# Kernel tuning notes

Hardware: AMD Instinct MI355X
Metric: run time of the kernel (lower is better)

The kernel has to match this reference:

```python
import jax, jax.numpy as jnp
import numpy as np

N = 100_000
E = 1_600_000
H = 128
L = 3
EPS = 1e-5


def setup_inputs() -> dict:
    key = jax.random.key(0)
    ks = jax.random.split(key, 8)
    x = jax.random.normal(ks[0], (N, H), dtype=jnp.float32)
    edge_index = jax.random.randint(ks[1], (2, E), 0, N, dtype=jnp.int64)
    edge_weight = jax.random.uniform(ks[2], (E,), dtype=jnp.float32)
    # per-layer params (all layers are H->H since in_dim == hidden)
    s = 1.0 / np.sqrt(H)
    lin_neigh_w = jax.random.uniform(ks[3], (L, H, H), minval=-s, maxval=s, dtype=jnp.float32)
    lin_root_w = jax.random.uniform(ks[4], (L, H, H), minval=-s, maxval=s, dtype=jnp.float32)
    lin_root_b = jax.random.uniform(ks[5], (L, H), minval=-s, maxval=s, dtype=jnp.float32)
    ln_w = jnp.ones((L, H), dtype=jnp.float32)
    ln_b = jnp.zeros((L, H), dtype=jnp.float32)
    return {"x": x, "edge_index": edge_index, "edge_weight": edge_weight,
            "lin_neigh_w": lin_neigh_w, "lin_root_w": lin_root_w,
            "lin_root_b": lin_root_b, "ln_w": ln_w, "ln_b": ln_b}


def _layer(h, src, dst, e_w, w_neigh, w_root, b_root, g, b):
    # message: m_ij = w_ij * x_j ; aggregate: scatter-add over dst, normalized by sum of weights
    msg = e_w[:, None] * h[src]                                    # [E, H]
    agg = jax.ops.segment_sum(msg, dst, num_segments=N)            # [N, H]
    sum_w = jnp.clip(jax.ops.segment_sum(e_w, dst, num_segments=N), 1.0, None)
    out = agg / sum_w[:, None]
    out = out @ w_neigh.T + h @ w_root.T + b_root                  # lin_neigh + lin_root
    out = jax.nn.relu(out)
    # per-node LayerNorm over feature dim
    mu = jnp.mean(out, axis=-1, keepdims=True)
    var = jnp.var(out, axis=-1, keepdims=True)
    out = (out - mu) * jax.lax.rsqrt(var + EPS) * g + b
    return out  # dropout: inference no-op


def reference(x, edge_index, edge_weight, lin_neigh_w, lin_root_w, lin_root_b, ln_w, ln_b):
    src, dst = edge_index[0], edge_index[1]
    h = x
    for l in range(L):
        h = _layer(h, src, dst, edge_weight, lin_neigh_w[l], lin_root_w[l],
                   lin_root_b[l], ln_w[l], ln_b[l])
    return h
```

## Files before the change

kernel.cpp:

```cpp
#include <hip/hip_runtime.h>
#include <hip/hip_fp16.h>

#define H 128
#define EPS 1e-5f
#define BCAP 6144

typedef __attribute__((ext_vector_type(8))) _Float16 half8;
typedef __attribute__((ext_vector_type(4))) float f32x4;

__device__ inline __half2 u2h2(unsigned u) { return __builtin_bit_cast(__half2, u); }
__device__ inline unsigned h22u(__half2 h) { return __builtin_bit_cast(unsigned, h); }

__global__ void convert_kernel(const float* __restrict__ x, unsigned* __restrict__ hx, int n4) {
    int i = blockIdx.x * 256 + threadIdx.x;
    if (i >= n4) return;
    float4 v = reinterpret_cast<const float4*>(x)[i];
    unsigned p0 = h22u(__floats2half2_rn(v.x, v.y));
    unsigned p1 = h22u(__floats2half2_rn(v.z, v.w));
    reinterpret_cast<uint2*>(hx)[i] = make_uint2(p0, p1);
}

__global__ __launch_bounds__(256) void bhist_kernel(const int* __restrict__ dst,
                                                    int* __restrict__ ghist, int E, int NB) {
    __shared__ int hist[512];
    int t = threadIdx.x;
    for (int i = t; i < NB; i += 256) hist[i] = 0;
    __syncthreads();
    int base = blockIdx.x * 8192 + t;
#pragma unroll
    for (int k = 0; k < 32; ++k) {
        int e = base + k * 256;
        if (e < E) atomicAdd(&hist[dst[e] >> 8], 1);
    }
    __syncthreads();
    for (int i = t; i < NB; i += 256)
        if (hist[i]) atomicAdd(&ghist[i], hist[i]);
}

__global__ __launch_bounds__(512) void bscan_kernel(const int* __restrict__ ghist,
                                                    int* __restrict__ bucket_base,
                                                    int* __restrict__ cursor,
                                                    int* __restrict__ row_start,
                                                    int NB, int E, int N) {
    __shared__ int lds[512];
    int t = threadIdx.x;
    int v = (t < NB) ? ghist[t] : 0;
    lds[t] = v;
    __syncthreads();
    for (int off = 1; off < 512; off <<= 1) {
        int u = (t >= off) ? lds[t - off] : 0;
        __syncthreads();
        lds[t] += u;
        __syncthreads();
    }
    int excl = lds[t] - v;
    if (t < NB) {
        bucket_base[t] = excl;
        cursor[t] = excl;
    }
    if (t == 0) {
        bucket_base[NB] = E;
        row_start[N] = E;
    }
}

__global__ __launch_bounds__(1024) void bucketize_kernel(const int* __restrict__ src,
                                                         const int* __restrict__ dst,
                                                         const float* __restrict__ ew,
                                                         int* __restrict__ cursor,
                                                         int2* __restrict__ ee, int E, int NB) {
    __shared__ int hist[512];
    __shared__ int scn[512];
    __shared__ int gbase[512];
    __shared__ int2 stage[8192];
    int t = threadIdx.x;
    for (int i = t; i < NB; i += 1024) hist[i] = 0;
    __syncthreads();

    int e0 = blockIdx.x * 8192;
    int bb[8], rk[8], pk[8], wb[8];
#pragma unroll
    for (int k = 0; k < 8; ++k) {
        int e = e0 + t + k * 1024;
        if (e < E) {
            int s = src[e], d = dst[e];
            bb[k] = d >> 8;
            pk[k] = s | ((d & 255) << 17);
            wb[k] = __float_as_int(ew[e]);
            rk[k] = atomicAdd(&hist[bb[k]], 1);
        } else {
            bb[k] = -1;
        }
    }
    __syncthreads();
    if (t < 512) scn[t] = (t < NB) ? hist[t] : 0;
    __syncthreads();
    for (int off = 1; off < 512; off <<= 1) {
        int u = 0;
        if (t < 512 && t >= off) u = scn[t - off];
        __syncthreads();
        if (t < 512) scn[t] += u;
        __syncthreads();
    }
    for (int i = t; i < NB; i += 1024) {
        int c = hist[i];
        if (c > 0) gbase[i] = atomicAdd(&cursor[i], c);
    }
#pragma unroll
    for (int k = 0; k < 8; ++k) {
        if (bb[k] >= 0) {
            int start = scn[bb[k]] - hist[bb[k]];
            stage[start + rk[k]] = make_int2(pk[k], wb[k]);
        }
    }
    __syncthreads();
    int wv = t >> 6, ln = t & 63;
    for (int bk = wv; bk < NB; bk += 16) {
        int c = hist[bk];
        if (c == 0) continue;
        int s0 = scn[bk] - c;
        int gb = gbase[bk];
        for (int i = ln; i < c; i += 64) ee[gb + i] = stage[s0 + i];
    }
}

__global__ __launch_bounds__(256) void bsort_kernel(int2* __restrict__ ee,
                                                    const int* __restrict__ bucket_base,
                                                    int* __restrict__ row_start, int N) {
    __shared__ int cnts[256];
    __shared__ int scv[256];
    __shared__ int prefs[256];
    __shared__ int2 out[BCAP];
    int b = blockIdx.x;
    int base = bucket_base[b], endb = bucket_base[b + 1];
    int cnt = endb - base;
    int t = threadIdx.x;
    cnts[t] = 0;
    __syncthreads();
    for (int i = base + t; i < endb; i += 256) atomicAdd(&cnts[(ee[i].x >> 17) & 255], 1);
    __syncthreads();
    scv[t] = cnts[t];
    __syncthreads();
    for (int off = 1; off < 256; off <<= 1) {
        int u = (t >= off) ? scv[t - off] : 0;
        __syncthreads();
        scv[t] += u;
        __syncthreads();
    }
    int pref = scv[t] - cnts[t];
    prefs[t] = pref;
    int node = (b << 8) + t;
    if (node < N) row_start[node] = base + pref;
    __syncthreads();
    cnts[t] = 0;
    __syncthreads();
    for (int i = base + t; i < endb; i += 256) {
        int2 r = ee[i];
        int dl = (r.x >> 17) & 255;
        int rkk = atomicAdd(&cnts[dl], 1);
        int slot = prefs[dl] + rkk;
        if (slot < BCAP) out[slot] = make_int2(r.x & 0x1FFFF, r.y);
    }
    __syncthreads();
    {
        int s0 = prefs[t], c = cnts[t];
        float sw = 0.f;
        for (int k = 0; k < c; ++k) sw += __int_as_float(out[s0 + k].y);
        sw = sw < 1.f ? 1.f : sw;
        float inv = 1.f / sw;
        for (int k = 0; k < c; ++k) {
            float w = __int_as_float(out[s0 + k].y) * inv;
            unsigned hb = (unsigned)__half_as_ushort(__float2half(w));
            out[s0 + k].y = (int)(hb | (hb << 16));
        }
    }
    __syncthreads();
    for (int i = t; i < cnt; i += 256) ee[base + i] = out[i];
}

__global__ __launch_bounds__(256) void agg_kernel(const unsigned short* __restrict__ hx,
                                                  const int* __restrict__ row_start,
                                                  const int2* __restrict__ ee,
                                                  unsigned short* __restrict__ aggb, int N) {
    int t = threadIdx.x;
    int node = blockIdx.x * 4 + (t >> 6);
    if (node >= N) return;
    int lane = t & 63, q = lane >> 4, jb = lane & 15;
    unsigned acc0 = 0, acc1 = 0, acc2 = 0, acc3 = 0;
    __half2 h0 = u2h2(0), h1 = u2h2(0), h2 = u2h2(0), h3 = u2h2(0);
    int rs = row_start[node], re = row_start[node + 1];
    int i = rs;
    for (; i + 8 <= re; i += 8) {
        int2 ea = ee[i + q];
        int2 eb = ee[i + 4 + q];
        uint4 ua = *reinterpret_cast<const uint4*>(hx + (size_t)ea.x * H + jb * 8);
        uint4 ub = *reinterpret_cast<const uint4*>(hx + (size_t)eb.x * H + jb * 8);
        __half2 wa = u2h2((unsigned)ea.y), wb = u2h2((unsigned)eb.y);
        h0 = __hfma2(u2h2(ua.x), wa, h0);
        h1 = __hfma2(u2h2(ua.y), wa, h1);
        h2 = __hfma2(u2h2(ua.z), wa, h2);
        h3 = __hfma2(u2h2(ua.w), wa, h3);
        h0 = __hfma2(u2h2(ub.x), wb, h0);
        h1 = __hfma2(u2h2(ub.y), wb, h1);
        h2 = __hfma2(u2h2(ub.z), wb, h2);
        h3 = __hfma2(u2h2(ub.w), wb, h3);
    }
    for (; i < re; i += 4) {
        int idx = i + q;
        int2 ea = (idx < re) ? ee[idx] : make_int2(0, 0);
        uint4 ua = *reinterpret_cast<const uint4*>(hx + (size_t)ea.x * H + jb * 8);
        __half2 wa = u2h2((unsigned)ea.y);
        h0 = __hfma2(u2h2(ua.x), wa, h0);
        h1 = __hfma2(u2h2(ua.y), wa, h1);
        h2 = __hfma2(u2h2(ua.z), wa, h2);
        h3 = __hfma2(u2h2(ua.w), wa, h3);
    }
    acc0 = h22u(h0); acc1 = h22u(h1); acc2 = h22u(h2); acc3 = h22u(h3);
#pragma unroll
    for (int off = 16; off <= 32; off <<= 1) {
        acc0 = h22u(__hadd2(u2h2(acc0), u2h2((unsigned)__shfl_xor((int)acc0, off))));
        acc1 = h22u(__hadd2(u2h2(acc1), u2h2((unsigned)__shfl_xor((int)acc1, off))));
        acc2 = h22u(__hadd2(u2h2(acc2), u2h2((unsigned)__shfl_xor((int)acc2, off))));
        acc3 = h22u(__hadd2(u2h2(acc3), u2h2((unsigned)__shfl_xor((int)acc3, off))));
    }
    if (q == 0) {
        uint4 r = make_uint4(acc0, acc1, acc2, acc3);
        *reinterpret_cast<uint4*>(aggb + (size_t)node * H + jb * 8) = r;
    }
}

__global__ __launch_bounds__(256, 2) void gemm_ln_mfma(
    const unsigned short* __restrict__ aggb, const unsigned short* __restrict__ hx,
    const float* __restrict__ Wn, const float* __restrict__ Wr,
    const float* __restrict__ br, const float* __restrict__ g,
    const float* __restrict__ b, unsigned short* __restrict__ hout,
    float* __restrict__ outf, int final_layer, int N) {
    __shared__ half8 Bfl[4096];

    int t = threadIdx.x;
    int w = t >> 6, lane = t & 63;
    int Mbase = blockIdx.x * 256;

#pragma unroll
    for (int it = 0; it < 16; ++it) {
        int f = it * 4 + w;
        int kt = f >> 3, nb = f & 7;
        int n = nb * 16 + (lane & 15);
        int kk = (kt & 3) * 32 + (lane >> 4) * 8;
        const float* wp = ((kt < 4) ? Wn : Wr) + (size_t)n * H + kk;
        float4 wa = *reinterpret_cast<const float4*>(wp);
        float4 wb = *reinterpret_cast<const float4*>(wp + 4);
        half8 sv;
        sv[0] = (_Float16)wa.x; sv[1] = (_Float16)wa.y;
        sv[2] = (_Float16)wa.z; sv[3] = (_Float16)wa.w;
        sv[4] = (_Float16)wb.x; sv[5] = (_Float16)wb.y;
        sv[6] = (_Float16)wb.z; sv[7] = (_Float16)wb.w;
        Bfl[f * 64 + lane] = sv;
    }
    __syncthreads();

    int lrow = lane & 15, lk = lane >> 4;
    const char* aggp = (const char*)aggb;
    const char* hp = (const char*)hx;
    size_t rb[4];
#pragma unroll
    for (int mf = 0; mf < 4; ++mf) {
        int r = Mbase + w * 64 + mf * 16 + lrow;
        r = r < N ? r : N - 1;
        rb[mf] = (size_t)r * 256;
    }

    f32x4 acc[4][8];
#pragma unroll
    for (int mf = 0; mf < 4; ++mf)
#pragma unroll
        for (int nb = 0; nb < 8; ++nb) acc[mf][nb] = (f32x4){0.f, 0.f, 0.f, 0.f};

#pragma unroll
    for (int kt = 0; kt < 8; ++kt) {
        const char* base = (kt < 4) ? aggp : hp;
        int off = (kt & 3) * 64 + lk * 16;
        half8 bf[8];
#pragma unroll
        for (int nb = 0; nb < 8; ++nb) bf[nb] = Bfl[(kt * 8 + nb) * 64 + lane];
#pragma unroll
        for (int mf = 0; mf < 4; ++mf) {
            half8 av = *reinterpret_cast<const half8*>(base + rb[mf] + off);
#pragma unroll
            for (int nb = 0; nb < 8; ++nb)
                acc[mf][nb] = __builtin_amdgcn_mfma_f32_16x16x32_f16(av, bf[nb], acc[mf][nb], 0, 0, 0);
        }
    }

    int col0 = lane & 15, rq = lane >> 4;
    float bias[8], gg[8], bbv[8];
#pragma unroll
    for (int nb = 0; nb < 8; ++nb) {
        int c = col0 + nb * 16;
        bias[nb] = br[c];
        gg[nb] = g[c];
        bbv[nb] = b[c];
    }
#pragma unroll
    for (int mf = 0; mf < 4; ++mf) {
#pragma unroll
        for (int reg = 0; reg < 4; ++reg) {
            float v[8];
            float s = 0.f, q = 0.f;
#pragma unroll
            for (int nb = 0; nb < 8; ++nb) {
                float u = acc[mf][nb][reg] + bias[nb];
                u = fmaxf(u, 0.f);
                v[nb] = u;
                s += u;
                q = fmaf(u, u, q);
            }
#pragma unroll
            for (int off = 1; off < 16; off <<= 1) {
                s += __shfl_xor(s, off);
                q += __shfl_xor(q, off);
            }
            float mu = s * (1.f / 128.f);
            float var = q * (1.f / 128.f) - mu * mu;
            float inv = rsqrtf(var + EPS);
            int grow = Mbase + w * 64 + mf * 16 + rq * 4 + reg;
            if (grow < N) {
                if (final_layer) {
#pragma unroll
                    for (int nb = 0; nb < 8; ++nb)
                        outf[(size_t)grow * H + col0 + nb * 16] = (v[nb] - mu) * inv * gg[nb] + bbv[nb];
                } else {
#pragma unroll
                    for (int nb = 0; nb < 8; ++nb)
                        hout[(size_t)grow * H + col0 + nb * 16] =
                            __half_as_ushort(__float2half((v[nb] - mu) * inv * gg[nb] + bbv[nb]));
                }
            }
        }
    }
}

static inline size_t alignup(size_t x) { return (x + 255) & ~(size_t)255; }

extern "C" void kernel_launch(void* const* d_in, const int* in_sizes, int n_in,
                              void* d_out, int out_size, void* d_ws, size_t ws_size,
                              hipStream_t stream) {
    const float* x  = (const float*)d_in[0];
    const int*   ei = (const int*)d_in[1];
    const float* ew = (const float*)d_in[2];
    const float* Wn = (const float*)d_in[3];
    const float* Wr = (const float*)d_in[4];
    const float* br = (const float*)d_in[5];
    const float* g  = (const float*)d_in[6];
    const float* bb = (const float*)d_in[7];
    float* out = (float*)d_out;

    int N = in_sizes[0] / H;
    int E = in_sizes[2];
    const int* src = ei;
    const int* dst = ei + E;
    int NB = (N + 255) >> 8;

    char* ws = (char*)d_ws;
    size_t off = 0;
    int* ghist = (int*)(ws + off);         off = alignup(off + sizeof(int) * 512);
    int* bucket_base = (int*)(ws + off);   off = alignup(off + sizeof(int) * 513);
    int* cursor = (int*)(ws + off);        off = alignup(off + sizeof(int) * 512);
    int* row_start = (int*)(ws + off);     off = alignup(off + sizeof(int) * ((size_t)N + 1));
    int2* ee = (int2*)(ws + off);          off = alignup(off + sizeof(int2) * (size_t)E);
    unsigned short* aggb = (unsigned short*)(ws + off); off = alignup(off + 2ull * N * H);
    unsigned short* hx = (unsigned short*)(ws + off);   off = alignup(off + 2ull * N * H);

    int eblocks = (E + 8191) / 8192;

    hipMemsetAsync(ghist, 0, sizeof(int) * 512, stream);
    bhist_kernel<<<eblocks, 256, 0, stream>>>(dst, ghist, E, NB);
    bscan_kernel<<<1, 512, 0, stream>>>(ghist, bucket_base, cursor, row_start, NB, E, N);
    bucketize_kernel<<<eblocks, 1024, 0, stream>>>(src, dst, ew, cursor, ee, E, NB);
    bsort_kernel<<<NB, 256, 0, stream>>>(ee, bucket_base, row_start, N);

    int n4 = N * H / 4;
    convert_kernel<<<(n4 + 255) / 256, 256, 0, stream>>>(x, (unsigned*)hx, n4);

    int gblocks = (N + 255) / 256;
    for (int l = 0; l < 3; ++l) {
        agg_kernel<<<(N + 3) / 4, 256, 0, stream>>>(hx, row_start, ee, aggb, N);
        gemm_ln_mfma<<<gblocks, 256, 0, stream>>>(
            aggb, hx,
            Wn + (size_t)l * H * H, Wr + (size_t)l * H * H, br + (size_t)l * H,
            g + (size_t)l * H, bb + (size_t)l * H,
            hx, out, (l == 2) ? 1 : 0, N);
    }
}
```

Baseline: 318.2 us.

## Pack edge records into 32-bit words and load four per lane

The sorted edge list is now written as one 32-bit word per edge: a 17-bit source index and a 15-bit truncated fp16 weight (sign bit dropped, low mantissa bit dropped). The aggregation kernel reads four packed records per lane with a single 16-byte load from an aligned start and masks out entries outside the node's range. The goal is to halve edge-index traffic across the three layers and issue fewer, wider loads. The cost is lower weight precision and loop iterations wasted on masked records, which still gather row 0 of the feature matrix.

```diff
diff --git a/kernel.cpp b/kernel.cpp
--- a/kernel.cpp
+++ b/kernel.cpp
@@ -124,9 +124,10 @@
     }
 }
 
-__global__ __launch_bounds__(256) void bsort_kernel(int2* __restrict__ ee,
+__global__ __launch_bounds__(256) void bsort_kernel(const int2* __restrict__ ee,
                                                     const int* __restrict__ bucket_base,
-                                                    int* __restrict__ row_start, int N) {
+                                                    int* __restrict__ row_start,
+                                                    unsigned* __restrict__ ee4, int N) {
     __shared__ int cnts[256];
     __shared__ int scv[256];
     __shared__ int prefs[256];
@@ -170,61 +171,52 @@
         float inv = 1.f / sw;
         for (int k = 0; k < c; ++k) {
             float w = __int_as_float(out[s0 + k].y) * inv;
-            unsigned hb = (unsigned)__half_as_ushort(__float2half(w));
-            out[s0 + k].y = (int)(hb | (hb << 16));
-        }
-    }
-    __syncthreads();
-    for (int i = t; i < cnt; i += 256) ee[base + i] = out[i];
+            out[s0 + k].y = (int)(unsigned)__half_as_ushort(__float2half(w));
+        }
+    }
+    __syncthreads();
+    for (int i = t; i < cnt; i += 256)
+        ee4[base + i] = ((unsigned)out[i].x << 15) | ((unsigned)out[i].y >> 1);
 }
 
 __global__ __launch_bounds__(256) void agg_kernel(const unsigned short* __restrict__ hx,
                                                   const int* __restrict__ row_start,
-                                                  const int2* __restrict__ ee,
+                                                  const unsigned* __restrict__ ee4,
                                                   unsigned short* __restrict__ aggb, int N) {
     int t = threadIdx.x;
     int node = blockIdx.x * 4 + (t >> 6);
     if (node >= N) return;
     int lane = t & 63, q = lane >> 4, jb = lane & 15;
-    unsigned acc0 = 0, acc1 = 0, acc2 = 0, acc3 = 0;
+    int rs = row_start[node], re = row_start[node + 1];
     __half2 h0 = u2h2(0), h1 = u2h2(0), h2 = u2h2(0), h3 = u2h2(0);
-    int rs = row_start[node], re = row_start[node + 1];
-    int i = rs;
-    for (; i + 8 <= re; i += 8) {
-        int2 ea = ee[i + q];
-        int2 eb = ee[i + 4 + q];
-        uint4 ua = *reinterpret_cast<const uint4*>(hx + (size_t)ea.x * H + jb * 8);
-        uint4 ub = *reinterpret_cast<const uint4*>(hx + (size_t)eb.x * H + jb * 8);
-        __half2 wa = u2h2((unsigned)ea.y), wb = u2h2((unsigned)eb.y);
-        h0 = __hfma2(u2h2(ua.x), wa, h0);
-        h1 = __hfma2(u2h2(ua.y), wa, h1);
-        h2 = __hfma2(u2h2(ua.z), wa, h2);
-        h3 = __hfma2(u2h2(ua.w), wa, h3);
-        h0 = __hfma2(u2h2(ub.x), wb, h0);
-        h1 = __hfma2(u2h2(ub.y), wb, h1);
-        h2 = __hfma2(u2h2(ub.z), wb, h2);
-        h3 = __hfma2(u2h2(ub.w), wb, h3);
-    }
-    for (; i < re; i += 4) {
-        int idx = i + q;
-        int2 ea = (idx < re) ? ee[idx] : make_int2(0, 0);
-        uint4 ua = *reinterpret_cast<const uint4*>(hx + (size_t)ea.x * H + jb * 8);
-        __half2 wa = u2h2((unsigned)ea.y);
-        h0 = __hfma2(u2h2(ua.x), wa, h0);
-        h1 = __hfma2(u2h2(ua.y), wa, h1);
-        h2 = __hfma2(u2h2(ua.z), wa, h2);
-        h3 = __hfma2(u2h2(ua.w), wa, h3);
-    }
-    acc0 = h22u(h0); acc1 = h22u(h1); acc2 = h22u(h2); acc3 = h22u(h3);
+    for (int i = (rs & ~3); i < re; i += 16) {
+        int rbase = i + q * 4;
+        uint4 rv = *reinterpret_cast<const uint4*>(ee4 + rbase);
+#pragma unroll
+        for (int k = 0; k < 4; ++k) {
+            unsigned rec = (k == 0) ? rv.x : (k == 1) ? rv.y : (k == 2) ? rv.z : rv.w;
+            int idx = rbase + k;
+            bool act = (idx >= rs) & (idx < re);
+            rec = act ? rec : 0u;
+            unsigned hw = (rec & 0x7FFFu) << 1;
+            __half2 w2 = u2h2(hw | (hw << 16));
+            unsigned srcv = rec >> 15;
+            uint4 hv = *reinterpret_cast<const uint4*>(hx + (size_t)srcv * H + jb * 8);
+            h0 = __hfma2(u2h2(hv.x), w2, h0);
+            h1 = __hfma2(u2h2(hv.y), w2, h1);
+            h2 = __hfma2(u2h2(hv.z), w2, h2);
+            h3 = __hfma2(u2h2(hv.w), w2, h3);
+        }
+    }
 #pragma unroll
     for (int off = 16; off <= 32; off <<= 1) {
-        acc0 = h22u(__hadd2(u2h2(acc0), u2h2((unsigned)__shfl_xor((int)acc0, off))));
-        acc1 = h22u(__hadd2(u2h2(acc1), u2h2((unsigned)__shfl_xor((int)acc1, off))));
-        acc2 = h22u(__hadd2(u2h2(acc2), u2h2((unsigned)__shfl_xor((int)acc2, off))));
-        acc3 = h22u(__hadd2(u2h2(acc3), u2h2((unsigned)__shfl_xor((int)acc3, off))));
+        h0 = __hadd2(h0, u2h2((unsigned)__shfl_xor((int)h22u(h0), off)));
+        h1 = __hadd2(h1, u2h2((unsigned)__shfl_xor((int)h22u(h1), off)));
+        h2 = __hadd2(h2, u2h2((unsigned)__shfl_xor((int)h22u(h2), off)));
+        h3 = __hadd2(h3, u2h2((unsigned)__shfl_xor((int)h22u(h3), off)));
     }
     if (q == 0) {
-        uint4 r = make_uint4(acc0, acc1, acc2, acc3);
+        uint4 r = make_uint4(h22u(h0), h22u(h1), h22u(h2), h22u(h3));
         *reinterpret_cast<uint4*>(aggb + (size_t)node * H + jb * 8) = r;
     }
 }
@@ -306,22 +298,22 @@
 #pragma unroll
         for (int reg = 0; reg < 4; ++reg) {
             float v[8];
-            float s = 0.f, q = 0.f;
+            float s = 0.f, qq = 0.f;
 #pragma unroll
             for (int nb = 0; nb < 8; ++nb) {
                 float u = acc[mf][nb][reg] + bias[nb];
                 u = fmaxf(u, 0.f);
                 v[nb] = u;
                 s += u;
-                q = fmaf(u, u, q);
+                qq = fmaf(u, u, qq);
             }
 #pragma unroll
             for (int off = 1; off < 16; off <<= 1) {
                 s += __shfl_xor(s, off);
-                q += __shfl_xor(q, off);
+                qq += __shfl_xor(qq, off);
             }
             float mu = s * (1.f / 128.f);
-            float var = q * (1.f / 128.f) - mu * mu;
+            float var = qq * (1.f / 128.f) - mu * mu;
             float inv = rsqrtf(var + EPS);
             int grow = Mbase + w * 64 + mf * 16 + rq * 4 + reg;
             if (grow < N) {
@@ -368,6 +360,7 @@
     int* cursor = (int*)(ws + off);        off = alignup(off + sizeof(int) * 512);
     int* row_start = (int*)(ws + off);     off = alignup(off + sizeof(int) * ((size_t)N + 1));
     int2* ee = (int2*)(ws + off);          off = alignup(off + sizeof(int2) * (size_t)E);
+    unsigned* ee4 = (unsigned*)(ws + off); off = alignup(off + sizeof(unsigned) * (size_t)E + 64);
     unsigned short* aggb = (unsigned short*)(ws + off); off = alignup(off + 2ull * N * H);
     unsigned short* hx = (unsigned short*)(ws + off);   off = alignup(off + 2ull * N * H);
 
@@ -377,14 +370,14 @@
     bhist_kernel<<<eblocks, 256, 0, stream>>>(dst, ghist, E, NB);
     bscan_kernel<<<1, 512, 0, stream>>>(ghist, bucket_base, cursor, row_start, NB, E, N);
     bucketize_kernel<<<eblocks, 1024, 0, stream>>>(src, dst, ew, cursor, ee, E, NB);
-    bsort_kernel<<<NB, 256, 0, stream>>>(ee, bucket_base, row_start, N);
+    bsort_kernel<<<NB, 256, 0, stream>>>(ee, bucket_base, row_start, ee4, N);
 
     int n4 = N * H / 4;
     convert_kernel<<<(n4 + 255) / 256, 256, 0, stream>>>(x, (unsigned*)hx, n4);
 
     int gblocks = (N + 255) / 256;
     for (int l = 0; l < 3; ++l) {
-        agg_kernel<<<(N + 3) / 4, 256, 0, stream>>>(hx, row_start, ee, aggb, N);
+        agg_kernel<<<(N + 3) / 4, 256, 0, stream>>>(hx, row_start, ee4, aggb, N);
         gemm_ln_mfma<<<gblocks, 256, 0, stream>>>(
             aggb, hx,
             Wn + (size_t)l * H * H, Wr + (size_t)l * H * H, br + (size_t)l * H,
```

New measurement: 306.5 us. 1.04x faster.
